# Kernel tuning notes

Measured on AMD Instinct MI355X. Metric: run time of the kernel, lower is better.

Reference implementation:

```python
import jax, jax.numpy as jnp
import numpy as np

RES_H, RES_W = 64, 64
INV_SMOOTHNESS = 0.1
OFFSET = 0.5
LOSS_WEIGHT = 1.0


def bilinear_sample(mask, xs, ys):
    # mask: [IH, IW]; xs: [Wo]; ys: [Ho] in pixel coords -> [Ho, Wo]
    IH, IW = mask.shape
    x0 = jnp.floor(xs); y0 = jnp.floor(ys)
    wx = xs - x0; wy = ys - y0
    x0i = jnp.clip(x0.astype(jnp.int32), 0, IW - 1)
    x1i = jnp.clip(x0i + 1, 0, IW - 1)
    y0i = jnp.clip(y0.astype(jnp.int32), 0, IH - 1)
    y1i = jnp.clip(y0i + 1, 0, IH - 1)
    g = lambda yi, xi: mask[yi[:, None], xi[None, :]]
    return ((1 - wy)[:, None] * ((1 - wx)[None, :] * g(y0i, x0i) + wx[None, :] * g(y0i, x1i))
            + wy[:, None] * ((1 - wx)[None, :] * g(y1i, x0i) + wx[None, :] * g(y1i, x1i)))


def crop_and_resize(masks, boxes, Ho, Wo):
    # masks: [N, IH, IW]; boxes: [N, 4] xyxy -> binarized [N, Ho, Wo]
    def one(mask, box):
        x1, y1, x2, y2 = box[0], box[1], box[2], box[3]
        xs = x1 + (x2 - x1) * (jnp.arange(Wo, dtype=masks.dtype) + 0.5) / Wo - 0.5
        ys = y1 + (y2 - y1) * (jnp.arange(Ho, dtype=masks.dtype) + 0.5) / Ho - 0.5
        return bilinear_sample(mask, xs, ys)
    out = jax.vmap(one)(masks, boxes)
    return (out >= 0.5).astype(masks.dtype)


def rasterize_mask(verts, H, W, inv_s):
    # Soft polygon rasterization, MODE_MASK: sigmoid(sign * min_sq_dist * inv_s).
    # verts: [N, V, 2] (x, y) in pixel coords of the HxW grid.
    N, V, _ = verts.shape
    xs = jnp.arange(W, dtype=verts.dtype)
    ys = jnp.arange(H, dtype=verts.dtype)
    px = jnp.tile(xs, H)       # [P] with P = H*W
    py = jnp.repeat(ys, W)     # [P]
    p = jnp.stack([px, py], -1)  # [P, 2]
    a = verts                          # [N, V, 2]
    b = jnp.roll(verts, -1, axis=1)    # next vertex (closed polygon)
    ab = b - a                         # [N, V, 2]
    denom = jnp.sum(ab * ab, -1)       # [N, V]
    pa = p[None, :, None, :] - a[:, None, :, :]            # [N, P, V, 2]
    t = jnp.clip(jnp.einsum('npvc,nvc->npv', pa, ab) / (denom[:, None, :] + 1e-12), 0.0, 1.0)
    diff = pa - t[..., None] * ab[:, None, :, :]
    d2 = jnp.sum(diff * diff, -1)      # [N, P, V] squared point-to-segment dist
    d2min = jnp.min(d2, -1)            # [N, P]
    # even-odd crossing test for inside/outside sign
    ay = a[..., 1][:, None, :]; by = b[..., 1][:, None, :]     # [N, 1, V]
    pyb = py[None, :, None]
    cond = (ay > pyb) != (by > pyb)                             # [N, P, V]
    dy = ab[..., 1][:, None, :]
    safe_dy = jnp.where(dy == 0, 1.0, dy)
    xint = a[..., 0][:, None, :] + (pyb - ay) * ab[..., 0][:, None, :] / safe_dy
    crossings = jnp.sum((cond & (px[None, :, None] < xint)).astype(jnp.int32), -1)  # [N, P]
    sign = jnp.where(crossings % 2 == 1, 1.0, -1.0)
    return jax.nn.sigmoid(sign * d2min * inv_s).reshape(N, H, W)


def dice_loss(inp, tgt):
    n = inp.shape[0]
    smooth = 1.0
    iflat = inp.reshape(n, -1)
    tflat = tgt.reshape(n, -1)
    inter = jnp.sum(iflat * tflat, -1)
    losses = 1.0 - (2.0 * inter + smooth) / (jnp.sum(iflat, -1) + jnp.sum(tflat, -1) + smooth)
    return jnp.sum(losses) / n


def setup_inputs() -> dict:
    key = jax.random.key(0)
    k1, k2, k3, k4, k5, k6 = jax.random.split(key, 6)
    N, V, IMG = 128, 128, 512
    # star-shaped polygons (realistic contours) in image coords
    ctr = jax.random.uniform(k1, (N, 1, 2)) * (IMG * 0.6) + IMG * 0.2
    ang = jnp.linspace(0.0, 2.0 * jnp.pi, V, endpoint=False)
    rad = 20.0 + jax.random.uniform(k2, (N, V)) * 60.0
    preds = ctr + jnp.stack([rad * jnp.cos(ang), rad * jnp.sin(ang)], -1)  # [N, V, 2]
    # gt boxes xyxy
    x1y1 = jax.random.uniform(k3, (N, 2)) * (IMG * 0.3)
    wh = 50.0 + jax.random.uniform(k4, (N, 2)) * (IMG * 0.4)
    targets_bboxes = jnp.concatenate([x1y1, x1y1 + wh], -1)  # [N, 4]
    # gt full-image masks: random disks
    cb = jax.random.uniform(k5, (N, 2)) * IMG
    r = 30.0 + jax.random.uniform(k6, (N,)) * 100.0
    yy = jnp.arange(IMG, dtype=jnp.float32)[None, :, None]
    xx = jnp.arange(IMG, dtype=jnp.float32)[None, None, :]
    targets_masks = (((xx - cb[:, 0, None, None]) ** 2 + (yy - cb[:, 1, None, None]) ** 2)
                     < (r[:, None, None] ** 2)).astype(jnp.float32)  # [N, IMG, IMG]
    return {"preds": preds, "targets_masks": targets_masks, "targets_bboxes": targets_bboxes}


def reference(preds, targets_masks, targets_bboxes):
    # union bboxes of predicted polygon extent and gt bbox
    pmin = jnp.min(preds, axis=1)
    pmax = jnp.max(preds, axis=1)
    ub = jnp.concatenate([jnp.minimum(pmin, targets_bboxes[:, :2]),
                          jnp.maximum(pmax, targets_bboxes[:, 2:4])], -1)  # [N, 4]
    # crop + resize + binarize gt masks at the union boxes
    tgt = crop_and_resize(targets_masks, ub, RES_H, RES_W)  # [N, 64, 64]
    # normalize polygons into the (detached) union box
    ubd = jax.lax.stop_gradient(ub)
    normed = (preds - ubd[:, None, :2]) / (ubd[:, None, 2:4] - ubd[:, None, :2])
    verts = normed * float(RES_W) - OFFSET
    pred_masks = rasterize_mask(verts, RES_H, RES_W, INV_SMOOTHNESS)  # [N, 64, 64]
    pred_masks = jnp.clip(pred_masks, 1e-5, 0.99999)
    return dice_loss(pred_masks, tgt) * LOSS_WEIGHT
```

## Files before the change

### kernel.cpp

```cpp
#include <hip/hip_runtime.h>
#include <hip/hip_bf16.h>

#define NMASK 128
#define NV    128
#define IMG   512
#define RES   64
#define PB    4
#define NBLK  (NMASK*PB)
#define BT    256

#define EDGES_OFF 0
#define UB_OFF    131072
#define ACC_OFF   131584
#define CNT_OFF   131968
#define FLAG_OFF  131969

__device__ __forceinline__ int clampi(int v, int lo, int hi) {
    return v < lo ? lo : (v > hi ? hi : v);
}

__device__ __forceinline__ int detect_bf16(const void* preds) {
    const __hip_bfloat16* pb = (const __hip_bfloat16*)preds;
    int lane = threadIdx.x & 63;
    float v = __bfloat162float(pb[2 * lane]);
    bool ok = (v >= 1.0f) && (v <= 600.0f);
    unsigned long long m = __ballot(ok);
    return (m == 0xFFFFFFFFFFFFFFFFULL) ? 1 : 0;
}

__device__ __forceinline__ float loadf(const void* p, long idx, int isb) {
    if (isb) return __bfloat162float(((const __hip_bfloat16*)p)[idx]);
    return ((const float*)p)[idx];
}

__global__ void __launch_bounds__(128) setup_kernel(
    const void* __restrict__ preds,
    const void* __restrict__ bboxes,
    float* __restrict__ ws)
{
    int n = blockIdx.x, t = threadIdx.x;
    int isb = detect_bf16(preds);

    float vx = loadf(preds, ((long)n*NV + t)*2 + 0, isb);
    float vy = loadf(preds, ((long)n*NV + t)*2 + 1, isb);

    float mnx = vx, mxx = vx, mny = vy, mxy = vy;
    for (int off = 32; off >= 1; off >>= 1) {
        mnx = fminf(mnx, __shfl_xor(mnx, off));
        mxx = fmaxf(mxx, __shfl_xor(mxx, off));
        mny = fminf(mny, __shfl_xor(mny, off));
        mxy = fmaxf(mxy, __shfl_xor(mxy, off));
    }
    __shared__ float r[2][4];
    int w = t >> 6;
    if ((t & 63) == 0) { r[w][0]=mnx; r[w][1]=mxx; r[w][2]=mny; r[w][3]=mxy; }
    __syncthreads();
    mnx = fminf(r[0][0], r[1][0]);
    mxx = fmaxf(r[0][1], r[1][1]);
    mny = fminf(r[0][2], r[1][2]);
    mxy = fmaxf(r[0][3], r[1][3]);

    float bx1 = loadf(bboxes, n*4 + 0, isb);
    float by1 = loadf(bboxes, n*4 + 1, isb);
    float bx2 = loadf(bboxes, n*4 + 2, isb);
    float by2 = loadf(bboxes, n*4 + 3, isb);
    float ux1 = fminf(mnx, bx1), uy1 = fminf(mny, by1);
    float ux2 = fmaxf(mxx, bx2), uy2 = fmaxf(mxy, by2);
    float sx = (float)RES / (ux2 - ux1);
    float sy = (float)RES / (uy2 - uy1);

    __shared__ float2 vn[NV];
    vn[t] = make_float2((vx - ux1)*sx - 0.5f, (vy - uy1)*sy - 0.5f);
    __syncthreads();

    float2 a = vn[t];
    float2 b = vn[(t + 1) & (NV - 1)];
    float abx = b.x - a.x, aby = b.y - a.y;
    float inv = 1.0f / (abx*abx + aby*aby + 1e-12f);
    float slope = abx / ((aby == 0.0f) ? 1.0f : aby);

    float4* eg = (float4*)(ws + EDGES_OFF + (size_t)n * NV * 8);
    eg[2*t]   = make_float4(a.x, a.y, abx, aby);
    eg[2*t+1] = make_float4(inv, slope, b.y, 0.0f);

    if (t == 0) {
        ws[UB_OFF + n*4 + 0] = ux1;
        ws[UB_OFF + n*4 + 1] = uy1;
        ws[UB_OFF + n*4 + 2] = ux2;
        ws[UB_OFF + n*4 + 3] = uy2;
        ws[ACC_OFF + n*3 + 0] = 0.0f;
        ws[ACC_OFF + n*3 + 1] = 0.0f;
        ws[ACC_OFF + n*3 + 2] = 0.0f;
        if (n == 0) {
            ((int*)ws)[CNT_OFF]  = 0;
            ((int*)ws)[FLAG_OFF] = isb;
        }
    }
}

__global__ void __launch_bounds__(BT) MaskRasterizationLoss_2705829396671_kernel(
    const void* __restrict__ masks,
    float* __restrict__ ws,
    void* __restrict__ out)
{
    int n    = blockIdx.x >> 2;
    int part = blockIdx.x & 3;
    int t    = threadIdx.x;

    __shared__ __align__(16) float4 eds[NV*2];
    __shared__ float red[3][4];
    __shared__ int   s_last;
    __shared__ float fin[2];

    const float4* eg = (const float4*)(ws + EDGES_OFF + (size_t)n * NV * 8);
    eds[t] = eg[t];

    float ux1 = ws[UB_OFF + n*4 + 0], uy1 = ws[UB_OFF + n*4 + 1];
    float ux2 = ws[UB_OFF + n*4 + 2], uy2 = ws[UB_OFF + n*4 + 3];
    int isb = ((const int*)ws)[FLAG_OFF];
    float* acc = ws + ACC_OFF;
    __syncthreads();

    int p0 = part * 1024 + t * 4;
    float py  = (float)(p0 >> 6);
    float pxb = (float)(p0 & 63);

    float d2m[4] = {1e30f, 1e30f, 1e30f, 1e30f};
    int   cr[4]  = {0, 0, 0, 0};

    #pragma unroll 4
    for (int v = 0; v < NV; ++v) {
        float4 e0 = eds[2*v];
        float4 e1 = eds[2*v+1];
        float pay  = py - e0.y;
        float q    = pay * e0.w;
        bool  cnd  = (e0.y > py) != (e1.z > py);
        float xint = fmaf(pay, e1.y, e0.x);
        #pragma unroll
        for (int k = 0; k < 4; ++k) {
            float px  = pxb + (float)k;
            float pax = px - e0.x;
            float tt  = fmaf(pax, e0.z, q) * e1.x;
            tt = fminf(fmaxf(tt, 0.0f), 1.0f);
            float dx  = fmaf(-tt, e0.z, pax);
            float dyv = fmaf(-tt, e0.w, pay);
            float d2  = fmaf(dx, dx, dyv*dyv);
            d2m[k] = fminf(d2m[k], d2);
            cr[k] ^= (cnd && (px < xint)) ? 1 : 0;
        }
    }

    long mbase = (long)n * IMG * IMG;
    float invW = (ux2 - ux1) * (1.0f/(float)RES);
    float invH = (uy2 - uy1) * (1.0f/(float)RES);
    float ys = fmaf(py + 0.5f, invH, uy1) - 0.5f;
    float fy = floorf(ys), wy = ys - fy;
    int y0i = clampi((int)fy, 0, IMG-1);
    int y1i = clampi(y0i + 1, 0, IMG-1);

    float s_pred = 0.0f, s_tgt = 0.0f, s_int = 0.0f;
    #pragma unroll
    for (int k = 0; k < 4; ++k) {
        float px = pxb + (float)k;
        float sgn = (cr[k] & 1) ? 1.0f : -1.0f;
        float z = sgn * d2m[k] * 0.1f;
        float sg = 1.0f / (1.0f + __expf(-z));
        sg = fminf(fmaxf(sg, 1e-5f), 0.99999f);

        float xs = fmaf(px + 0.5f, invW, ux1) - 0.5f;
        float fx = floorf(xs), wx = xs - fx;
        int x0i = clampi((int)fx, 0, IMG-1);
        int x1i = clampi(x0i + 1, 0, IMG-1);
        float g00 = loadf(masks, mbase + (long)y0i*IMG + x0i, isb);
        float g01 = loadf(masks, mbase + (long)y0i*IMG + x1i, isb);
        float g10 = loadf(masks, mbase + (long)y1i*IMG + x0i, isb);
        float g11 = loadf(masks, mbase + (long)y1i*IMG + x1i, isb);
        float bil = (1.0f-wy) * ((1.0f-wx)*g00 + wx*g01)
                  +        wy * ((1.0f-wx)*g10 + wx*g11);
        float tg = (bil >= 0.5f) ? 1.0f : 0.0f;

        s_pred += sg;
        s_tgt  += tg;
        s_int  += sg * tg;
    }

    for (int off = 32; off >= 1; off >>= 1) {
        s_pred += __shfl_xor(s_pred, off);
        s_tgt  += __shfl_xor(s_tgt,  off);
        s_int  += __shfl_xor(s_int,  off);
    }
    int wave = t >> 6;
    if ((t & 63) == 0) { red[0][wave]=s_pred; red[1][wave]=s_tgt; red[2][wave]=s_int; }
    __syncthreads();
    if (t == 0) {
        atomicAdd(&acc[n*3+0], red[0][0]+red[0][1]+red[0][2]+red[0][3]);
        atomicAdd(&acc[n*3+1], red[1][0]+red[1][1]+red[1][2]+red[1][3]);
        atomicAdd(&acc[n*3+2], red[2][0]+red[2][1]+red[2][2]+red[2][3]);
        __threadfence();
        int old = atomicAdd((int*)ws + CNT_OFF, 1);
        s_last = (old == NBLK - 1) ? 1 : 0;
    }
    __syncthreads();

    if (s_last) {
        __threadfence();
        float loss = 0.0f;
        if (t < NMASK) {
            float sp = atomicAdd(&acc[t*3+0], 0.0f);
            float st = atomicAdd(&acc[t*3+1], 0.0f);
            float si = atomicAdd(&acc[t*3+2], 0.0f);
            loss = 1.0f - (2.0f*si + 1.0f) / (sp + st + 1.0f);
        }
        for (int off = 32; off >= 1; off >>= 1)
            loss += __shfl_xor(loss, off);
        if (t == 0)  fin[0] = loss;
        if (t == 64) fin[1] = loss;
        __syncthreads();
        if (t == 0) {
            float L = (fin[0] + fin[1]) * (1.0f/(float)NMASK);
            unsigned int fb = __float_as_uint(L);
            unsigned int r  = (fb + 0x7FFFu + ((fb >> 16) & 1u)) >> 16;
            ((unsigned int*)out)[0] = (r << 16) | r;
        }
    }
}

extern "C" void kernel_launch(void* const* d_in, const int* in_sizes, int n_in,
                              void* d_out, int out_size, void* d_ws, size_t ws_size,
                              hipStream_t stream) {
    const void* preds  = d_in[0];
    const void* masks  = d_in[1];
    const void* bboxes = d_in[2];
    float* ws = (float*)d_ws;

    setup_kernel<<<NMASK, 128, 0, stream>>>(preds, bboxes, ws);
    MaskRasterizationLoss_2705829396671_kernel<<<NBLK, BT, 0, stream>>>(masks, ws, d_out);
}
```

Baseline: 211.2 us.

## Double block count, read edges from global, split finalize into separate kernel

Each mask is now split across 8 blocks with 2 pixels per thread instead of 4 blocks with 4 pixels, doubling the grid to raise parallelism. Edge data is read directly from global memory instead of being staged in LDS, which drops the block-level sync. The last-block counter and fence logic is replaced by a separate single-block finalize kernel. The risks are less per-thread reuse of edge loads, more global or cache traffic per pixel, and an extra kernel launch.

```diff
diff --git a/kernel.cpp b/kernel.cpp
--- a/kernel.cpp
+++ b/kernel.cpp
@@ -5,15 +5,14 @@
 #define NV    128
 #define IMG   512
 #define RES   64
-#define PB    4
+#define PB    8
 #define NBLK  (NMASK*PB)
 #define BT    256
 
 #define EDGES_OFF 0
 #define UB_OFF    131072
 #define ACC_OFF   131584
-#define CNT_OFF   131968
-#define FLAG_OFF  131969
+#define FLAG_OFF  131968
 
 __device__ __forceinline__ int clampi(int v, int lo, int hi) {
     return v < lo ? lo : (v > hi ? hi : v);
@@ -91,62 +90,63 @@
         ws[ACC_OFF + n*3 + 0] = 0.0f;
         ws[ACC_OFF + n*3 + 1] = 0.0f;
         ws[ACC_OFF + n*3 + 2] = 0.0f;
-        if (n == 0) {
-            ((int*)ws)[CNT_OFF]  = 0;
-            ((int*)ws)[FLAG_OFF] = isb;
-        }
+        if (n == 0) ((int*)ws)[FLAG_OFF] = isb;
     }
 }
 
 __global__ void __launch_bounds__(BT) MaskRasterizationLoss_2705829396671_kernel(
     const void* __restrict__ masks,
-    float* __restrict__ ws,
-    void* __restrict__ out)
+    const float4* __restrict__ edges,
+    const float* __restrict__ meta,
+    float* __restrict__ acc)
 {
-    int n    = blockIdx.x >> 2;
-    int part = blockIdx.x & 3;
+    int n    = blockIdx.x >> 3;
+    int part = blockIdx.x & 7;
     int t    = threadIdx.x;
 
-    __shared__ __align__(16) float4 eds[NV*2];
-    __shared__ float red[3][4];
-    __shared__ int   s_last;
-    __shared__ float fin[2];
-
-    const float4* eg = (const float4*)(ws + EDGES_OFF + (size_t)n * NV * 8);
-    eds[t] = eg[t];
-
-    float ux1 = ws[UB_OFF + n*4 + 0], uy1 = ws[UB_OFF + n*4 + 1];
-    float ux2 = ws[UB_OFF + n*4 + 2], uy2 = ws[UB_OFF + n*4 + 3];
-    int isb = ((const int*)ws)[FLAG_OFF];
-    float* acc = ws + ACC_OFF;
-    __syncthreads();
-
-    int p0 = part * 1024 + t * 4;
+    const float4* eg = edges + (size_t)n * NV * 2;
+
+    float ux1 = meta[UB_OFF + n*4 + 0], uy1 = meta[UB_OFF + n*4 + 1];
+    float ux2 = meta[UB_OFF + n*4 + 2], uy2 = meta[UB_OFF + n*4 + 3];
+    int isb = ((const int*)meta)[FLAG_OFF];
+
+    int p0 = part * 512 + t * 2;
     float py  = (float)(p0 >> 6);
     float pxb = (float)(p0 & 63);
-
-    float d2m[4] = {1e30f, 1e30f, 1e30f, 1e30f};
-    int   cr[4]  = {0, 0, 0, 0};
-
-    #pragma unroll 4
+    float px1v = pxb + 1.0f;
+
+    float d2m0 = 1e30f, d2m1 = 1e30f;
+    int   cr0 = 0, cr1 = 0;
+
+    #pragma unroll 8
     for (int v = 0; v < NV; ++v) {
-        float4 e0 = eds[2*v];
-        float4 e1 = eds[2*v+1];
-        float pay  = py - e0.y;
-        float q    = pay * e0.w;
-        bool  cnd  = (e0.y > py) != (e1.z > py);
-        float xint = fmaf(pay, e1.y, e0.x);
-        #pragma unroll
-        for (int k = 0; k < 4; ++k) {
-            float px  = pxb + (float)k;
-            float pax = px - e0.x;
-            float tt  = fmaf(pax, e0.z, q) * e1.x;
+        float4 eA = eg[2*v];
+        float4 eB = eg[2*v+1];
+
+        float pay  = py - eA.y;
+        float q    = pay * eA.w;
+        bool  cnd  = (eA.y > py) != (eB.z > py);
+        float xint = fmaf(pay, eB.y, eA.x);
+
+        {
+            float pax = pxb - eA.x;
+            float tt  = fmaf(pax, eA.z, q) * eB.x;
             tt = fminf(fmaxf(tt, 0.0f), 1.0f);
-            float dx  = fmaf(-tt, e0.z, pax);
-            float dyv = fmaf(-tt, e0.w, pay);
+            float dx  = fmaf(-tt, eA.z, pax);
+            float dyv = fmaf(-tt, eA.w, pay);
             float d2  = fmaf(dx, dx, dyv*dyv);
-            d2m[k] = fminf(d2m[k], d2);
-            cr[k] ^= (cnd && (px < xint)) ? 1 : 0;
+            d2m0 = fminf(d2m0, d2);
+            cr0 += (cnd && (pxb < xint)) ? 1 : 0;
+        }
+        {
+            float pax = px1v - eA.x;
+            float tt  = fmaf(pax, eA.z, q) * eB.x;
+            tt = fminf(fmaxf(tt, 0.0f), 1.0f);
+            float dx  = fmaf(-tt, eA.z, pax);
+            float dyv = fmaf(-tt, eA.w, pay);
+            float d2  = fmaf(dx, dx, dyv*dyv);
+            d2m1 = fminf(d2m1, d2);
+            cr1 += (cnd && (px1v < xint)) ? 1 : 0;
         }
     }
 
@@ -160,10 +160,13 @@
 
     float s_pred = 0.0f, s_tgt = 0.0f, s_int = 0.0f;
     #pragma unroll
-    for (int k = 0; k < 4; ++k) {
-        float px = pxb + (float)k;
-        float sgn = (cr[k] & 1) ? 1.0f : -1.0f;
-        float z = sgn * d2m[k] * 0.1f;
+    for (int k = 0; k < 2; ++k) {
+        float px    = k ? px1v : pxb;
+        float d2min = k ? d2m1 : d2m0;
+        int   cross = k ? cr1  : cr0;
+
+        float sgn = (cross & 1) ? 1.0f : -1.0f;
+        float z = sgn * d2min * 0.1f;
         float sg = 1.0f / (1.0f + __expf(-z));
         sg = fminf(fmaxf(sg, 1e-5f), 0.99999f);
 
@@ -189,6 +192,7 @@
         s_tgt  += __shfl_xor(s_tgt,  off);
         s_int  += __shfl_xor(s_int,  off);
     }
+    __shared__ float red[3][4];
     int wave = t >> 6;
     if ((t & 63) == 0) { red[0][wave]=s_pred; red[1][wave]=s_tgt; red[2][wave]=s_int; }
     __syncthreads();
@@ -196,32 +200,25 @@
         atomicAdd(&acc[n*3+0], red[0][0]+red[0][1]+red[0][2]+red[0][3]);
         atomicAdd(&acc[n*3+1], red[1][0]+red[1][1]+red[1][2]+red[1][3]);
         atomicAdd(&acc[n*3+2], red[2][0]+red[2][1]+red[2][2]+red[2][3]);
-        __threadfence();
-        int old = atomicAdd((int*)ws + CNT_OFF, 1);
-        s_last = (old == NBLK - 1) ? 1 : 0;
-    }
-    __syncthreads();
-
-    if (s_last) {
-        __threadfence();
-        float loss = 0.0f;
-        if (t < NMASK) {
-            float sp = atomicAdd(&acc[t*3+0], 0.0f);
-            float st = atomicAdd(&acc[t*3+1], 0.0f);
-            float si = atomicAdd(&acc[t*3+2], 0.0f);
-            loss = 1.0f - (2.0f*si + 1.0f) / (sp + st + 1.0f);
-        }
-        for (int off = 32; off >= 1; off >>= 1)
-            loss += __shfl_xor(loss, off);
-        if (t == 0)  fin[0] = loss;
-        if (t == 64) fin[1] = loss;
-        __syncthreads();
-        if (t == 0) {
-            float L = (fin[0] + fin[1]) * (1.0f/(float)NMASK);
-            unsigned int fb = __float_as_uint(L);
-            unsigned int r  = (fb + 0x7FFFu + ((fb >> 16) & 1u)) >> 16;
-            ((unsigned int*)out)[0] = (r << 16) | r;
-        }
+    }
+}
+
+__global__ void __launch_bounds__(128) finalize_kernel(
+    const float* __restrict__ acc, void* __restrict__ out)
+{
+    int t = threadIdx.x;
+    float sp = acc[t*3+0], st = acc[t*3+1], si = acc[t*3+2];
+    float loss = 1.0f - (2.0f*si + 1.0f) / (sp + st + 1.0f);
+    for (int off = 32; off >= 1; off >>= 1)
+        loss += __shfl_xor(loss, off);
+    __shared__ float tmp[2];
+    if ((t & 63) == 0) tmp[t >> 6] = loss;
+    __syncthreads();
+    if (t == 0) {
+        float L = (tmp[0] + tmp[1]) * (1.0f/128.0f);
+        unsigned int fb = __float_as_uint(L);
+        unsigned int r  = (fb + 0x7FFFu + ((fb >> 16) & 1u)) >> 16;
+        ((unsigned int*)out)[0] = (r << 16) | r;
     }
 }
 
@@ -234,5 +231,7 @@
     float* ws = (float*)d_ws;
 
     setup_kernel<<<NMASK, 128, 0, stream>>>(preds, bboxes, ws);
-    MaskRasterizationLoss_2705829396671_kernel<<<NBLK, BT, 0, stream>>>(masks, ws, d_out);
-}
+    MaskRasterizationLoss_2705829396671_kernel<<<NBLK, BT, 0, stream>>>(
+        masks, (const float4*)(ws + EDGES_OFF), ws, ws + ACC_OFF);
+    finalize_kernel<<<1, 128, 0, stream>>>(ws + ACC_OFF, d_out);
+}
```

Result: faster. 192.5 us (-8.8%).
